# Kernel tuning notes

Hardware: AMD Instinct MI355X
Metric: run time of the kernel (lower is better)

The kernel has to match this reference:

```python
import jax, jax.numpy as jnp
import numpy as np

# Problem-size constants (match input_specs / init_kwargs)
B, D, H, W = 2, 128, 128, 128   # batch and spatial grid
N = 200_000                      # number of active (non-empty) voxels
CI, CO, K = 64, 64, 3            # channels and cubic kernel size
DIL = 1                          # dilation


def setup_inputs() -> dict:
    key = jax.random.key(0)
    k1, k2, k3 = jax.random.split(key, 3)
    # Unique active voxel coordinates (submanifold conv assumes unique sites).
    rng = np.random.default_rng(0)
    lin = rng.choice(B * D * H * W, size=N, replace=False)
    b, rem = np.divmod(lin, D * H * W)
    z, rem = np.divmod(rem, H * W)
    y, x = np.divmod(rem, W)
    coords = jnp.asarray(np.stack([b, z, y, x], axis=1).astype(np.int32))  # [N,4]
    feats = jax.random.normal(k1, (N, CI), dtype=jnp.float32)
    # kaiming-uniform-ish init, layout [Co, Kd, Kh, Kw, Ci] as in the module
    fan_in = CI * K * K * K
    bound = 1.0 / np.sqrt(fan_in)
    weight = jax.random.uniform(k2, (CO, K, K, K, CI), dtype=jnp.float32,
                                minval=-bound, maxval=bound)
    bias = jax.random.uniform(k3, (CO,), dtype=jnp.float32,
                              minval=-bound, maxval=bound)
    return {"feats": feats, "weight": weight, "bias": bias, "coords": coords}


def _build_grid(coords):
    """Dense voxel hash: linear cell id -> row index in feats (-1 if empty)."""
    n = coords.shape[0]
    lin = ((coords[:, 0] * D + coords[:, 1]) * H + coords[:, 2]) * W + coords[:, 3]
    grid = jnp.full((B * D * H * W,), -1, dtype=jnp.int32)
    return grid.at[lin].set(jnp.arange(n, dtype=jnp.int32))


def reference(feats, weight, bias, coords):
    # Submanifold sparse 3D conv: out[p] = bias + sum_k W[k] @ feats[p + dil*(k - center)]
    # (only where the neighbor voxel is active; output sites == input sites).
    n = feats.shape[0]
    grid = _build_grid(coords)
    c = K // 2
    bz, z0, y0, x0 = coords[:, 0], coords[:, 1], coords[:, 2], coords[:, 3]
    out = jnp.broadcast_to(bias.astype(feats.dtype), (n, CO))
    for kd in range(K):
        for kh in range(K):
            for kw in range(K):
                dz, dy, dx = DIL * (kd - c), DIL * (kh - c), DIL * (kw - c)
                nz, ny, nx = z0 + dz, y0 + dy, x0 + dx
                inb = (nz >= 0) & (nz < D) & (ny >= 0) & (ny < H) & (nx >= 0) & (nx < W)
                nlin = ((bz * D + jnp.clip(nz, 0, D - 1)) * H
                        + jnp.clip(ny, 0, H - 1)) * W + jnp.clip(nx, 0, W - 1)
                nidx = jnp.where(inb, grid[nlin], -1)          # rulebook for this offset
                valid = (nidx >= 0)[:, None]
                g = jnp.where(valid, feats[jnp.clip(nidx, 0)], 0.0)  # gather [N,Ci]
                out = out + jnp.einsum('nc,oc->no', g, weight[:, kd, kh, kw, :])
    return out
```

## Files before the change

kernel.cpp:

```cpp
#include <hip/hip_runtime.h>
#include <hip/hip_bf16.h>

#define BDIM 2
#define DDIM 128
#define HDIM 128
#define WDIM 128
#define CI 64
#define CO 64
#define NTAPS 27
#define GRID_CELLS (BDIM * DDIM * HDIM * WDIM)
#define NCBLK (GRID_CELLS / 256)

typedef __attribute__((ext_vector_type(8))) short short8;
typedef __attribute__((ext_vector_type(4))) float floatx4;

#define WT_OFF   ((size_t)16 << 20)
#define BCNT_OFF (WT_OFF + ((size_t)256 << 10))
#define ORD_OFF  (BCNT_OFF + ((size_t)64 << 10))
#define ZROW_OFF (ORD_OFF + ((size_t)1 << 20))
#define FB_OFF   ((size_t)18 << 20)

typedef const __attribute__((address_space(1))) void* gas_t;
typedef __attribute__((address_space(3))) void* las_t;

__device__ __forceinline__ unsigned short f2bf(float f) {
    unsigned int u = __float_as_uint(f);
    return (unsigned short)((u + 0x7FFFu + ((u >> 16) & 1u)) >> 16);
}

__global__ __launch_bounds__(256) void setup_kernel(
    const int* __restrict__ coords, int* __restrict__ grid, int n,
    const float* __restrict__ weight, short8* __restrict__ wt8,
    float* __restrict__ zrow, const float* __restrict__ feats,
    short8* __restrict__ fb8, int nbf) {
    int bid = blockIdx.x, tid = threadIdx.x;
    if (bid < 54) {
        int idx = bid * 256 + tid;
        int l = idx & 63, ot = (idx >> 6) & 3, s = (idx >> 8) & 1, t = idx >> 9;
        int o = ot * 16 + (l & 15);
        int k0 = s * 32 + ((l >> 4) << 3);
        const float* src = weight + ((size_t)o * NTAPS + t) * CI + k0;
        short8 v;
#pragma unroll
        for (int j = 0; j < 8; ++j) v[j] = (short)f2bf(src[j]);
        wt8[idx] = v;
    } else if (bid == 54) {
        if (tid < 64) zrow[tid] = 0.f;
    } else if (bid < 55 + nbf) {
        int g = (bid - 55) * 256 + tid;
        if (g < n * 8) {
            const float* s = feats + (size_t)g * 8;
            short8 v;
#pragma unroll
            for (int j = 0; j < 8; ++j) v[j] = (short)f2bf(s[j]);
            fb8[g] = v;
        }
    } else {
        int i = (bid - 55 - nbf) * 256 + tid;
        if (i < n) {
            int4 c = ((const int4*)coords)[i];
            grid[((c.x * DDIM + c.y) * HDIM + c.z) * WDIM + c.w] = i;
        }
    }
}

__global__ __launch_bounds__(256) void count_kernel(
    const int* __restrict__ grid, int* __restrict__ bcnt) {
    int i = blockIdx.x * 256 + threadIdx.x;
    unsigned long long b = __ballot(grid[i] >= 0);
    __shared__ int wc[4];
    if ((threadIdx.x & 63) == 0) wc[threadIdx.x >> 6] = __popcll(b);
    __syncthreads();
    if (threadIdx.x == 0) bcnt[blockIdx.x] = wc[0] + wc[1] + wc[2] + wc[3];
}

__global__ __launch_bounds__(1024) void scan_kernel(int* __restrict__ bcnt) {
    __shared__ int part[1024];
    int tid = threadIdx.x;
    int v[16], s = 0;
#pragma unroll
    for (int k = 0; k < 16; ++k) { v[k] = bcnt[tid * 16 + k]; s += v[k]; }
    part[tid] = s;
    __syncthreads();
    for (int off = 1; off < 1024; off <<= 1) {
        int t = (tid >= off) ? part[tid - off] : 0;
        __syncthreads();
        part[tid] += t;
        __syncthreads();
    }
    int ex = tid ? part[tid - 1] : 0;
#pragma unroll
    for (int k = 0; k < 16; ++k) { int nv = ex; ex += v[k]; bcnt[tid * 16 + k] = nv; }
}

__global__ __launch_bounds__(256) void emit_kernel(
    const int* __restrict__ grid, const int* __restrict__ boff,
    int* __restrict__ order) {
    int i = blockIdx.x * 256 + threadIdx.x;
    int v = grid[i];
    int lane = threadIdx.x & 63, w = threadIdx.x >> 6;
    unsigned long long b = __ballot(v >= 0);
    __shared__ int wc[4];
    if (lane == 0) wc[w] = __popcll(b);
    __syncthreads();
    int woff = 0;
    for (int k = 0; k < w; ++k) woff += wc[k];
    if (v >= 0) {
        int rank = __popcll(b & ((1ull << lane) - 1ull));
        order[boff[blockIdx.x] + woff + rank] = v;
    }
}

template <bool BF>
__global__ __launch_bounds__(256) void conv_kernel(
    const float* __restrict__ feats, const short8* __restrict__ fb8,
    const short8* __restrict__ wt8, const float* __restrict__ bias,
    const int* __restrict__ coords, const int* __restrict__ grid,
    const int* __restrict__ order, const float* __restrict__ zrow,
    float* __restrict__ out, int n) {
    __shared__ short8 bs[4][512];
    int tid = threadIdx.x;
    int w = tid >> 6, l = tid & 63, quad = l >> 4, m = l & 15;

    float b0 = bias[m], b1 = bias[m + 16], b2 = bias[m + 32], b3 = bias[m + 48];

    int jrow = blockIdx.x * 64 + w * 16 + m;
    int j = jrow < n ? jrow : n - 1;
    int p = order[j];
    int4 c = ((const int4*)coords)[p];

    int pr[7];
#pragma unroll
    for (int i = 0; i < 7; ++i) {
        int t = 4 * i + quad;
        int v = -1;
        if (t < NTAPS) {
            int dz = t / 9 - 1, rem = t % 9;
            int dy = rem / 3 - 1, dx = rem % 3 - 1;
            int nz = c.y + dz, ny = c.z + dy, nx = c.w + dx;
            if (nz >= 0 && nz < DDIM && ny >= 0 && ny < HDIM &&
                nx >= 0 && nx < WDIM)
                v = grid[((c.x * DDIM + nz) * HDIM + ny) * WDIM + nx];
        }
        pr[i] = v;
    }

    floatx4 acc0 = {0.f, 0.f, 0.f, 0.f}, acc1 = acc0, acc2 = acc0, acc3 = acc0;
    short8 xb[3][2];
    float4 xf[3][4];
    int vval[3];

#define VMW(N) asm volatile("s_waitcnt vmcnt(" #N ")" ::: "memory")

#define STAGE(t)                                                              \
    {                                                                         \
        const short8* gsrc = wt8 + (size_t)(t) * 512 + w * 128 + l;           \
        __builtin_amdgcn_global_load_lds((gas_t)gsrc,                         \
            (las_t)&bs[(t) & 3][w * 128], 16, 0, 0);                          \
        __builtin_amdgcn_global_load_lds((gas_t)(gsrc + 64),                  \
            (las_t)&bs[(t) & 3][w * 128 + 64], 16, 0, 0);                     \
    }

#define GATHER(t)                                                             \
    {                                                                         \
        int vv = __shfl(pr[(t) >> 2], (((t) & 3) << 4) | m);                  \
        vval[(t) % 3] = vv;                                                   \
        if constexpr (BF) {                                                   \
            const short8* ar =                                                \
                (vv >= 0 ? fb8 + (size_t)vv * 8 : (const short8*)zrow) + quad;\
            xb[(t) % 3][0] = ar[0];                                           \
            xb[(t) % 3][1] = ar[4];                                           \
        } else {                                                              \
            const float4* ar =                                                \
                (const float4*)(vv >= 0 ? feats + (size_t)vv * CI : zrow) +   \
                quad * 2;                                                     \
            float4* xp = xf[(t) % 3];                                         \
            xp[0] = ar[0]; xp[1] = ar[1]; xp[2] = ar[8]; xp[3] = ar[9];       \
        }                                                                     \
    }

#define COMPUTE(t)                                                                 \
    if (__ballot(vval[(t) % 3] >= 0) != 0ull) {                                    \
        short8 f0s, f1s;                                                           \
        if constexpr (BF) {                                                        \
            f0s = xb[(t) % 3][0];                                                  \
            f1s = xb[(t) % 3][1];                                                  \
        } else {                                                                   \
            const float4* g = xf[(t) % 3];                                         \
            union { short8 s; __hip_bfloat162 h[4]; } f0, f1;                      \
            f0.h[0] = __float22bfloat162_rn({g[0].x, g[0].y});                     \
            f0.h[1] = __float22bfloat162_rn({g[0].z, g[0].w});                     \
            f0.h[2] = __float22bfloat162_rn({g[1].x, g[1].y});                     \
            f0.h[3] = __float22bfloat162_rn({g[1].z, g[1].w});                     \
            f1.h[0] = __float22bfloat162_rn({g[2].x, g[2].y});                     \
            f1.h[1] = __float22bfloat162_rn({g[2].z, g[2].w});                     \
            f1.h[2] = __float22bfloat162_rn({g[3].x, g[3].y});                     \
            f1.h[3] = __float22bfloat162_rn({g[3].z, g[3].w});                     \
            f0s = f0.s; f1s = f1.s;                                                \
        }                                                                          \
        const short8* wb = &bs[(t) & 3][l];                                        \
        __builtin_amdgcn_s_setprio(1);                                             \
        acc0 = __builtin_amdgcn_mfma_f32_16x16x32_bf16(f0s, wb[0 * 64], acc0, 0, 0, 0); \
        acc1 = __builtin_amdgcn_mfma_f32_16x16x32_bf16(f0s, wb[1 * 64], acc1, 0, 0, 0); \
        acc2 = __builtin_amdgcn_mfma_f32_16x16x32_bf16(f0s, wb[2 * 64], acc2, 0, 0, 0); \
        acc3 = __builtin_amdgcn_mfma_f32_16x16x32_bf16(f0s, wb[3 * 64], acc3, 0, 0, 0); \
        acc0 = __builtin_amdgcn_mfma_f32_16x16x32_bf16(f1s, wb[4 * 64], acc0, 0, 0, 0); \
        acc1 = __builtin_amdgcn_mfma_f32_16x16x32_bf16(f1s, wb[5 * 64], acc1, 0, 0, 0); \
        acc2 = __builtin_amdgcn_mfma_f32_16x16x32_bf16(f1s, wb[6 * 64], acc2, 0, 0, 0); \
        acc3 = __builtin_amdgcn_mfma_f32_16x16x32_bf16(f1s, wb[7 * 64], acc3, 0, 0, 0); \
        __builtin_amdgcn_s_setprio(0);                                             \
    }

    STAGE(0); GATHER(0);
    STAGE(1); GATHER(1);

#pragma unroll
    for (int t = 0; t < NTAPS; ++t) {
        if (t + 2 < NTAPS) { STAGE(t + 2); GATHER(t + 2); }
        if constexpr (BF) {
            if (t < NTAPS - 2)       { VMW(8); }
            else if (t == NTAPS - 2) { VMW(4); }
            else                     { VMW(0); }
        } else {
            if (t < NTAPS - 2)       { VMW(12); }
            else if (t == NTAPS - 2) { VMW(6); }
            else                     { VMW(0); }
        }
        __builtin_amdgcn_sched_barrier(0);
        __builtin_amdgcn_s_barrier();
        __builtin_amdgcn_sched_barrier(0);
        COMPUTE(t);
        __builtin_amdgcn_sched_barrier(0);
    }

#pragma unroll
    for (int r = 0; r < 4; ++r) {
        int row = quad * 4 + r;
        int jr = blockIdx.x * 64 + w * 16 + row;
        int prow = __shfl(p, row);
        if (jr < n) {
            float* orow = out + (size_t)prow * CO;
            orow[m]      = acc0[r] + b0;
            orow[m + 16] = acc1[r] + b1;
            orow[m + 32] = acc2[r] + b2;
            orow[m + 48] = acc3[r] + b3;
        }
    }
#undef STAGE
#undef GATHER
#undef COMPUTE
#undef VMW
}

extern "C" void kernel_launch(void* const* d_in, const int* in_sizes, int n_in,
                              void* d_out, int out_size, void* d_ws, size_t ws_size,
                              hipStream_t stream) {
    const float* feats  = (const float*)d_in[0];
    const float* weight = (const float*)d_in[1];
    const float* bias   = (const float*)d_in[2];
    const int*   coords = (const int*)d_in[3];
    float* out = (float*)d_out;
    int n = in_sizes[3] / 4;

    int*    grid  = (int*)d_ws;
    short8* wt8   = (short8*)((char*)d_ws + WT_OFF);
    int*    bcnt  = (int*)((char*)d_ws + BCNT_OFF);
    int*    order = (int*)((char*)d_ws + ORD_OFF);
    float*  zrow  = (float*)((char*)d_ws + ZROW_OFF);
    short8* fb8   = (short8*)((char*)d_ws + FB_OFF);

    int useBF = ws_size >= FB_OFF + (size_t)n * CI * 2;
    int nbf = useBF ? (n * 8 + 255) / 256 : 0;

    (void)hipMemsetAsync(grid, 0xFF, (size_t)GRID_CELLS * sizeof(int), stream);
    setup_kernel<<<55 + nbf + (n + 255) / 256, 256, 0, stream>>>(
        coords, grid, n, weight, wt8, zrow, feats, fb8, nbf);
    count_kernel<<<NCBLK, 256, 0, stream>>>(grid, bcnt);
    scan_kernel<<<1, 1024, 0, stream>>>(bcnt);
    emit_kernel<<<NCBLK, 256, 0, stream>>>(grid, bcnt, order);
    if (useBF)
        conv_kernel<true><<<(n + 63) / 64, 256, 0, stream>>>(
            feats, fb8, wt8, bias, coords, grid, order, zrow, out, n);
    else
        conv_kernel<false><<<(n + 63) / 64, 256, 0, stream>>>(
            feats, fb8, wt8, bias, coords, grid, order, zrow, out, n);
}
```

Measured before the change: 191.8 us.

## Process two 16-row tiles per wave to reuse staged weights across more rows

Result: no change. 192.7 us (+0.5%).

```diff
diff --git a/kernel.cpp b/kernel.cpp
--- a/kernel.cpp
+++ b/kernel.cpp
@@ -121,18 +121,19 @@
     __shared__ short8 bs[4][512];
     int tid = threadIdx.x;
     int w = tid >> 6, l = tid & 63, quad = l >> 4, m = l & 15;
+    int half = l >> 5, q2 = (l >> 4) & 1;
 
     float b0 = bias[m], b1 = bias[m + 16], b2 = bias[m + 32], b3 = bias[m + 48];
 
-    int jrow = blockIdx.x * 64 + w * 16 + m;
+    int jrow = blockIdx.x * 128 + w * 32 + half * 16 + m;
     int j = jrow < n ? jrow : n - 1;
     int p = order[j];
     int4 c = ((const int4*)coords)[p];
 
-    int pr[7];
-#pragma unroll
-    for (int i = 0; i < 7; ++i) {
-        int t = 4 * i + quad;
+    int pr[14];
+#pragma unroll
+    for (int i = 0; i < 14; ++i) {
+        int t = 2 * i + q2;
         int v = -1;
         if (t < NTAPS) {
             int dz = t / 9 - 1, rem = t % 9;
@@ -145,10 +146,15 @@
         pr[i] = v;
     }
 
-    floatx4 acc0 = {0.f, 0.f, 0.f, 0.f}, acc1 = acc0, acc2 = acc0, acc3 = acc0;
-    short8 xb[3][2];
-    float4 xf[3][4];
-    int vval[3];
+    floatx4 acc[2][4];
+#pragma unroll
+    for (int a = 0; a < 2; ++a)
+#pragma unroll
+        for (int q = 0; q < 4; ++q) acc[a][q] = floatx4{0.f, 0.f, 0.f, 0.f};
+
+    short8 xb[3][2][2];
+    float4 xf[3][2][4];
+    int vval[3][2];
 
 #define VMW(N) asm volatile("s_waitcnt vmcnt(" #N ")" ::: "memory")
 
@@ -161,32 +167,33 @@
             (las_t)&bs[(t) & 3][w * 128 + 64], 16, 0, 0);                     \
     }
 
-#define GATHER(t)                                                             \
+#define GATHER1(t, a)                                                         \
     {                                                                         \
-        int vv = __shfl(pr[(t) >> 2], (((t) & 3) << 4) | m);                  \
-        vval[(t) % 3] = vv;                                                   \
+        int vv = __shfl(pr[(t) >> 1], ((a) << 5) | (((t) & 1) << 4) | m);     \
+        vval[(t) % 3][a] = vv;                                                \
         if constexpr (BF) {                                                   \
             const short8* ar =                                                \
                 (vv >= 0 ? fb8 + (size_t)vv * 8 : (const short8*)zrow) + quad;\
-            xb[(t) % 3][0] = ar[0];                                           \
-            xb[(t) % 3][1] = ar[4];                                           \
+            xb[(t) % 3][a][0] = ar[0];                                        \
+            xb[(t) % 3][a][1] = ar[4];                                        \
         } else {                                                              \
             const float4* ar =                                                \
                 (const float4*)(vv >= 0 ? feats + (size_t)vv * CI : zrow) +   \
                 quad * 2;                                                     \
-            float4* xp = xf[(t) % 3];                                         \
+            float4* xp = xf[(t) % 3][a];                                      \
             xp[0] = ar[0]; xp[1] = ar[1]; xp[2] = ar[8]; xp[3] = ar[9];       \
         }                                                                     \
     }
-
-#define COMPUTE(t)                                                                 \
-    if (__ballot(vval[(t) % 3] >= 0) != 0ull) {                                    \
+#define GATHER(t) { GATHER1(t, 0); GATHER1(t, 1); }
+
+#define COMPUTE1(t, a)                                                             \
+    if (__ballot(vval[(t) % 3][a] >= 0) != 0ull) {                                 \
         short8 f0s, f1s;                                                           \
         if constexpr (BF) {                                                        \
-            f0s = xb[(t) % 3][0];                                                  \
-            f1s = xb[(t) % 3][1];                                                  \
+            f0s = xb[(t) % 3][a][0];                                               \
+            f1s = xb[(t) % 3][a][1];                                               \
         } else {                                                                   \
-            const float4* g = xf[(t) % 3];                                         \
+            const float4* g = xf[(t) % 3][a];                                      \
             union { short8 s; __hip_bfloat162 h[4]; } f0, f1;                      \
             f0.h[0] = __float22bfloat162_rn({g[0].x, g[0].y});                     \
             f0.h[1] = __float22bfloat162_rn({g[0].z, g[0].w});                     \
@@ -200,16 +207,17 @@
         }                                                                          \
         const short8* wb = &bs[(t) & 3][l];                                        \
         __builtin_amdgcn_s_setprio(1);                                             \
-        acc0 = __builtin_amdgcn_mfma_f32_16x16x32_bf16(f0s, wb[0 * 64], acc0, 0, 0, 0); \
-        acc1 = __builtin_amdgcn_mfma_f32_16x16x32_bf16(f0s, wb[1 * 64], acc1, 0, 0, 0); \
-        acc2 = __builtin_amdgcn_mfma_f32_16x16x32_bf16(f0s, wb[2 * 64], acc2, 0, 0, 0); \
-        acc3 = __builtin_amdgcn_mfma_f32_16x16x32_bf16(f0s, wb[3 * 64], acc3, 0, 0, 0); \
-        acc0 = __builtin_amdgcn_mfma_f32_16x16x32_bf16(f1s, wb[4 * 64], acc0, 0, 0, 0); \
-        acc1 = __builtin_amdgcn_mfma_f32_16x16x32_bf16(f1s, wb[5 * 64], acc1, 0, 0, 0); \
-        acc2 = __builtin_amdgcn_mfma_f32_16x16x32_bf16(f1s, wb[6 * 64], acc2, 0, 0, 0); \
-        acc3 = __builtin_amdgcn_mfma_f32_16x16x32_bf16(f1s, wb[7 * 64], acc3, 0, 0, 0); \
+        acc[a][0] = __builtin_amdgcn_mfma_f32_16x16x32_bf16(f0s, wb[0 * 64], acc[a][0], 0, 0, 0); \
+        acc[a][1] = __builtin_amdgcn_mfma_f32_16x16x32_bf16(f0s, wb[1 * 64], acc[a][1], 0, 0, 0); \
+        acc[a][2] = __builtin_amdgcn_mfma_f32_16x16x32_bf16(f0s, wb[2 * 64], acc[a][2], 0, 0, 0); \
+        acc[a][3] = __builtin_amdgcn_mfma_f32_16x16x32_bf16(f0s, wb[3 * 64], acc[a][3], 0, 0, 0); \
+        acc[a][0] = __builtin_amdgcn_mfma_f32_16x16x32_bf16(f1s, wb[4 * 64], acc[a][0], 0, 0, 0); \
+        acc[a][1] = __builtin_amdgcn_mfma_f32_16x16x32_bf16(f1s, wb[5 * 64], acc[a][1], 0, 0, 0); \
+        acc[a][2] = __builtin_amdgcn_mfma_f32_16x16x32_bf16(f1s, wb[6 * 64], acc[a][2], 0, 0, 0); \
+        acc[a][3] = __builtin_amdgcn_mfma_f32_16x16x32_bf16(f1s, wb[7 * 64], acc[a][3], 0, 0, 0); \
         __builtin_amdgcn_s_setprio(0);                                             \
     }
+#define COMPUTE(t) { COMPUTE1(t, 0); COMPUTE1(t, 1); }
 
     STAGE(0); GATHER(0);
     STAGE(1); GATHER(1);
@@ -218,12 +226,12 @@
     for (int t = 0; t < NTAPS; ++t) {
         if (t + 2 < NTAPS) { STAGE(t + 2); GATHER(t + 2); }
         if constexpr (BF) {
-            if (t < NTAPS - 2)       { VMW(8); }
-            else if (t == NTAPS - 2) { VMW(4); }
+            if (t < NTAPS - 2)       { VMW(12); }
+            else if (t == NTAPS - 2) { VMW(6); }
             else                     { VMW(0); }
         } else {
-            if (t < NTAPS - 2)       { VMW(12); }
-            else if (t == NTAPS - 2) { VMW(6); }
+            if (t < NTAPS - 2)       { VMW(20); }
+            else if (t == NTAPS - 2) { VMW(10); }
             else                     { VMW(0); }
         }
         __builtin_amdgcn_sched_barrier(0);
@@ -234,21 +242,25 @@
     }
 
 #pragma unroll
-    for (int r = 0; r < 4; ++r) {
-        int row = quad * 4 + r;
-        int jr = blockIdx.x * 64 + w * 16 + row;
-        int prow = __shfl(p, row);
-        if (jr < n) {
-            float* orow = out + (size_t)prow * CO;
-            orow[m]      = acc0[r] + b0;
-            orow[m + 16] = acc1[r] + b1;
-            orow[m + 32] = acc2[r] + b2;
-            orow[m + 48] = acc3[r] + b3;
-        }
-    }
+    for (int a = 0; a < 2; ++a)
+#pragma unroll
+        for (int r = 0; r < 4; ++r) {
+            int rr = quad * 4 + r;
+            int jr = blockIdx.x * 128 + w * 32 + a * 16 + rr;
+            int prow = __shfl(p, (a << 5) | rr);
+            if (jr < n) {
+                float* orow = out + (size_t)prow * CO;
+                orow[m]      = acc[a][0][r] + b0;
+                orow[m + 16] = acc[a][1][r] + b1;
+                orow[m + 32] = acc[a][2][r] + b2;
+                orow[m + 48] = acc[a][3][r] + b3;
+            }
+        }
 #undef STAGE
 #undef GATHER
+#undef GATHER1
 #undef COMPUTE
+#undef COMPUTE1
 #undef VMW
 }
 
@@ -279,9 +291,9 @@
     scan_kernel<<<1, 1024, 0, stream>>>(bcnt);
     emit_kernel<<<NCBLK, 256, 0, stream>>>(grid, bcnt, order);
     if (useBF)
-        conv_kernel<true><<<(n + 63) / 64, 256, 0, stream>>>(
+        conv_kernel<true><<<(n + 127) / 128, 256, 0, stream>>>(
             feats, fb8, wt8, bias, coords, grid, order, zrow, out, n);
     else
-        conv_kernel<false><<<(n + 63) / 64, 256, 0, stream>>>(
+        conv_kernel<false><<<(n + 127) / 128, 256, 0, stream>>>(
             feats, fb8, wt8, bias, coords, grid, order, zrow, out, n);
 }
```

## Fuse grid build, count, scan and emit into one cooperative kernel

Applied to the files above, without the earlier changes.

Measured after the change: 616.3 us. +221.3%, slower.

```diff
diff --git a/kernel.cpp b/kernel.cpp
--- a/kernel.cpp
+++ b/kernel.cpp
@@ -1,5 +1,8 @@
 #include <hip/hip_runtime.h>
 #include <hip/hip_bf16.h>
+#include <hip/hip_cooperative_groups.h>
+
+namespace cg = cooperative_groups;
 
 #define BDIM 2
 #define DDIM 128
@@ -10,6 +13,8 @@
 #define NTAPS 27
 #define GRID_CELLS (BDIM * DDIM * HDIM * WDIM)
 #define NCBLK (GRID_CELLS / 256)
+#define NB 1024
+#define CPB (NCBLK / NB)
 
 typedef __attribute__((ext_vector_type(8))) short short8;
 typedef __attribute__((ext_vector_type(4))) float floatx4;
@@ -26,6 +31,100 @@
 __device__ __forceinline__ unsigned short f2bf(float f) {
     unsigned int u = __float_as_uint(f);
     return (unsigned short)((u + 0x7FFFu + ((u >> 16) & 1u)) >> 16);
+}
+
+__global__ __launch_bounds__(256, 4) void pre_kernel(
+    const int* __restrict__ coords, int* __restrict__ grid, int n,
+    const float* __restrict__ weight, short8* __restrict__ wt8,
+    float* __restrict__ zrow, const float* __restrict__ feats,
+    short8* __restrict__ fb8, int* __restrict__ bcnt,
+    int* __restrict__ order, int useBF) {
+    cg::grid_group gg = cg::this_grid();
+    int b = blockIdx.x, tid = threadIdx.x;
+    int lane = tid & 63, wv = tid >> 6;
+
+    {
+        int4* g4 = (int4*)grid;
+        int base = b * 1024;
+#pragma unroll
+        for (int k = 0; k < 4; ++k)
+            g4[base + k * 256 + tid] = int4{-1, -1, -1, -1};
+    }
+    if (b < 54) {
+        int idx = b * 256 + tid;
+        int l = idx & 63, ot = (idx >> 6) & 3, s = (idx >> 8) & 1, t = idx >> 9;
+        int o = ot * 16 + (l & 15);
+        int k0 = s * 32 + ((l >> 4) << 3);
+        const float* src = weight + ((size_t)o * NTAPS + t) * CI + k0;
+        short8 v;
+#pragma unroll
+        for (int j = 0; j < 8; ++j) v[j] = (short)f2bf(src[j]);
+        wt8[idx] = v;
+    }
+    if (b == 54 && tid < 64) zrow[tid] = 0.f;
+    if (useBF) {
+        for (int g = b * 256 + tid; g < n * 8; g += NB * 256) {
+            const float* s = feats + (size_t)g * 8;
+            short8 v;
+#pragma unroll
+            for (int j = 0; j < 8; ++j) v[j] = (short)f2bf(s[j]);
+            fb8[g] = v;
+        }
+    }
+    gg.sync();
+
+    for (int i = b * 256 + tid; i < n; i += NB * 256) {
+        int4 c = ((const int4*)coords)[i];
+        grid[((c.x * DDIM + c.y) * HDIM + c.z) * WDIM + c.w] = i;
+    }
+    gg.sync();
+
+    int gv[CPB];
+    __shared__ int wcs[CPB][4];
+#pragma unroll
+    for (int k = 0; k < CPB; ++k) {
+        gv[k] = grid[(b * CPB + k) * 256 + tid];
+        unsigned long long bl = __ballot(gv[k] >= 0);
+        if (lane == 0) wcs[k][wv] = __popcll(bl);
+    }
+    __syncthreads();
+    if (tid < CPB)
+        bcnt[b * CPB + tid] =
+            wcs[tid][0] + wcs[tid][1] + wcs[tid][2] + wcs[tid][3];
+    gg.sync();
+
+    if (b == 0) {
+        __shared__ int part[256];
+        int s = 0;
+        for (int j = 0; j < 64; ++j) s += bcnt[tid * 64 + j];
+        part[tid] = s;
+        __syncthreads();
+        for (int off = 1; off < 256; off <<= 1) {
+            int t2 = (tid >= off) ? part[tid - off] : 0;
+            __syncthreads();
+            part[tid] += t2;
+            __syncthreads();
+        }
+        int ex = tid ? part[tid - 1] : 0;
+        for (int j = 0; j < 64; ++j) {
+            int v2 = bcnt[tid * 64 + j];
+            bcnt[tid * 64 + j] = ex;
+            ex += v2;
+        }
+    }
+    gg.sync();
+
+#pragma unroll
+    for (int k = 0; k < CPB; ++k) {
+        int v = gv[k];
+        unsigned long long bl = __ballot(v >= 0);
+        int woff = 0;
+        for (int w2 = 0; w2 < wv; ++w2) woff += wcs[k][w2];
+        if (v >= 0) {
+            int rank = __popcll(bl & ((1ull << lane) - 1ull));
+            order[bcnt[b * CPB + k] + woff + rank] = v;
+        }
+    }
 }
 
 __global__ __launch_bounds__(256) void setup_kernel(
@@ -270,14 +369,22 @@
     short8* fb8   = (short8*)((char*)d_ws + FB_OFF);
 
     int useBF = ws_size >= FB_OFF + (size_t)n * CI * 2;
-    int nbf = useBF ? (n * 8 + 255) / 256 : 0;
-
-    (void)hipMemsetAsync(grid, 0xFF, (size_t)GRID_CELLS * sizeof(int), stream);
-    setup_kernel<<<55 + nbf + (n + 255) / 256, 256, 0, stream>>>(
-        coords, grid, n, weight, wt8, zrow, feats, fb8, nbf);
-    count_kernel<<<NCBLK, 256, 0, stream>>>(grid, bcnt);
-    scan_kernel<<<1, 1024, 0, stream>>>(bcnt);
-    emit_kernel<<<NCBLK, 256, 0, stream>>>(grid, bcnt, order);
+
+    void* args[] = {(void*)&coords, (void*)&grid, (void*)&n, (void*)&weight,
+                    (void*)&wt8,    (void*)&zrow, (void*)&feats, (void*)&fb8,
+                    (void*)&bcnt,   (void*)&order, (void*)&useBF};
+    hipError_t ce = hipLaunchCooperativeKernel(
+        (void*)pre_kernel, dim3(NB), dim3(256), args, 0, stream);
+    if (ce != hipSuccess) {
+        int nbf = useBF ? (n * 8 + 255) / 256 : 0;
+        (void)hipMemsetAsync(grid, 0xFF, (size_t)GRID_CELLS * sizeof(int), stream);
+        setup_kernel<<<55 + nbf + (n + 255) / 256, 256, 0, stream>>>(
+            coords, grid, n, weight, wt8, zrow, feats, fb8, nbf);
+        count_kernel<<<NCBLK, 256, 0, stream>>>(grid, bcnt);
+        scan_kernel<<<1, 1024, 0, stream>>>(bcnt);
+        emit_kernel<<<NCBLK, 256, 0, stream>>>(grid, bcnt, order);
+    }
+
     if (useBF)
         conv_kernel<true><<<(n + 63) / 64, 256, 0, stream>>>(
             feats, fb8, wt8, bias, coords, grid, order, zrow, out, n);
```
